# Performance work log

Measured on AMD Instinct MI355X. Metric: run time of the kernel, lower is better.

The kernel has to match this reference:

```python
import jax, jax.numpy as jnp
import numpy as np

ALPHA = 32.0 ** 2
EPS = 1e-5
SCALE = 64 ** (-0.5)  # dim_head ** -0.5
HEADS = 8


def stable_softmax(t, alpha=ALPHA):
    t = t / alpha
    t = t - jax.lax.stop_gradient(jnp.max(t, axis=-1, keepdims=True))
    return jax.nn.softmax(t * alpha, axis=-1)


def setup_inputs() -> dict:
    key = jax.random.key(0)
    k1, k2, k3 = jax.random.split(key, 3)
    dim, inner = 512, 8 * 64
    x = jax.random.normal(k1, (8, dim, 32, 32), dtype=jnp.float32)
    gamma = jnp.ones((1, dim, 1, 1), dtype=jnp.float32)
    # conv2d 1x1 weights, stored as [out_ch, in_ch]
    w_qkv = jax.random.normal(k2, (inner * 3, dim), dtype=jnp.float32) * (dim ** -0.5)
    w_out = jax.random.normal(k3, (dim, inner), dtype=jnp.float32) * (inner ** -0.5)
    return {"x": x, "gamma": gamma, "w_qkv": w_qkv, "w_out": w_out}


def reference(x, gamma, w_qkv, w_out):
    b, c, H, W = x.shape
    residual = x
    # LayerNormChan: normalize over channel dim (biased variance), scale by gamma
    mean = jnp.mean(x, axis=1, keepdims=True)
    var = jnp.var(x, axis=1, keepdims=True)
    xn = (x - mean) / jnp.sqrt(var + EPS) * gamma
    # 1x1 conv QKV projection
    qkv = jnp.einsum('oc,bchw->bohw', w_qkv, xn)
    q, k, v = jnp.split(qkv, 3, axis=1)
    n = H * W
    def to_heads(t):
        return t.reshape(b, HEADS, -1, n)  # b h c (x y)
    q, k, v = map(to_heads, (q, k, v))
    sim = jnp.einsum('bhci,bhcj->bhij', q, k) * SCALE
    attn = stable_softmax(sim)
    out = jnp.einsum('bhij,bhcj->bhci', attn, v)
    out = out.reshape(b, -1, H, W)  # b (h c) x y
    out = jnp.einsum('oc,bchw->bohw', w_out, out)
    return out + residual
```

## Files before the change

kernel.cpp:

```cpp
#include <hip/hip_runtime.h>
#include <hip/hip_bf16.h>

#define NDIM   512
#define NPOS   1024
#define NB     8
#define INNER  1536
#define DHEAD  64

typedef __attribute__((ext_vector_type(8))) short bf8v;
typedef __attribute__((ext_vector_type(4))) float f4v;

__device__ __forceinline__ f4v mfma16(bf8v a, bf8v b, f4v c) {
    return __builtin_amdgcn_mfma_f32_16x16x32_bf16(a, b, c, 0, 0, 0);
}

__device__ __forceinline__ unsigned short f2bs(float v) {
    __hip_bfloat16 h = __float2bfloat16(v);
    return *reinterpret_cast<unsigned short*>(&h);
}

__global__ __launch_bounds__(256) void ln_xnorm_kernel(
    const float* __restrict__ x, const float* __restrict__ gamma,
    unsigned short* __restrict__ xnT)
{
    __shared__ float ssum[4][64];
    __shared__ float ssq[4][64];
    __shared__ float mean_s[64];
    __shared__ float rstd_s[64];
    __shared__ unsigned short tile[64][72];

    const int b = blockIdx.y;
    const int n0 = blockIdx.x * 64;
    const int t = threadIdx.x;

    {
        const int ln = t & 63, cg = t >> 6;
        const float* xp = x + (size_t)b * NDIM * NPOS + n0 + ln;
        float s = 0.f, ss = 0.f;
        for (int c = cg * 128; c < cg * 128 + 128; ++c) {
            float v = xp[(size_t)c * NPOS];
            s += v; ss += v * v;
        }
        ssum[cg][ln] = s; ssq[cg][ln] = ss;
    }
    __syncthreads();
    if (t < 64) {
        float st = ssum[0][t] + ssum[1][t] + ssum[2][t] + ssum[3][t];
        float sq = ssq[0][t] + ssq[1][t] + ssq[2][t] + ssq[3][t];
        float m = st * (1.0f / NDIM);
        float var = sq * (1.0f / NDIM) - m * m;
        mean_s[t] = m;
        rstd_s[t] = rsqrtf(var + 1e-5f);
    }
    __syncthreads();

    const int cl = t >> 2, nq = (t & 3) * 16;
    const int n = t >> 2, cq = (t & 3) * 16;
    for (int c0 = 0; c0 < NDIM; c0 += 64) {
        const float g = gamma[c0 + cl];
        const float* xp = x + ((size_t)b * NDIM + c0 + cl) * NPOS + n0 + nq;
#pragma unroll
        for (int q = 0; q < 4; ++q) {
            float4 v = *(const float4*)(xp + q * 4);
            float4 m = *(const float4*)&mean_s[nq + q * 4];
            float4 r = *(const float4*)&rstd_s[nq + q * 4];
            tile[nq + q * 4 + 0][cl] = f2bs((v.x - m.x) * r.x * g);
            tile[nq + q * 4 + 1][cl] = f2bs((v.y - m.y) * r.y * g);
            tile[nq + q * 4 + 2][cl] = f2bs((v.z - m.z) * r.z * g);
            tile[nq + q * 4 + 3][cl] = f2bs((v.w - m.w) * r.w * g);
        }
        __syncthreads();
        unsigned short* dst = xnT + ((size_t)b * NPOS + n0 + n) * NDIM + c0 + cq;
        *(uint4*)dst       = *(const uint4*)&tile[n][cq];
        *(uint4*)(dst + 8) = *(const uint4*)&tile[n][cq + 8];
        __syncthreads();
    }
}

__global__ __launch_bounds__(256) void castw2_kernel(
    const float* __restrict__ wq, unsigned short* __restrict__ wqb,
    const float* __restrict__ wo, unsigned short* __restrict__ wob)
{
    const int n1 = INNER * NDIM / 4;
    int i = blockIdx.x * 256 + threadIdx.x;
    const float* src; unsigned short* dst; int j;
    if (i < n1) { src = wq; dst = wqb; j = i; }
    else        { src = wo; dst = wob; j = i - n1; }
    float4 v = ((const float4*)src)[j];
    ushort4 u;
    u.x = f2bs(v.x); u.y = f2bs(v.y); u.z = f2bs(v.z); u.w = f2bs(v.w);
    ((ushort4*)dst)[j] = u;
}

__global__ __launch_bounds__(256) void qkv_mfma_kernel(
    const unsigned short* __restrict__ wq, const unsigned short* __restrict__ xnT,
    unsigned short* __restrict__ qT, unsigned short* __restrict__ kT,
    unsigned short* __restrict__ vv)
{
    __shared__ unsigned short smem[4 * 64 * 72];
    unsigned short (*Al)[40] = (unsigned short(*)[40])smem;
    unsigned short (*Bl)[40] = (unsigned short(*)[40])(smem + 5120);

    const int b = blockIdx.z;
    const int m0 = blockIdx.y * 128, n0 = blockIdx.x * 128;
    const int t = threadIdx.x, w = t >> 6, lane = t & 63;
    const int l15 = lane & 15, quad = lane >> 4;
    const int wm = (w >> 1) * 64, wn = (w & 1) * 64;
    const unsigned short* Abase = wq + (size_t)m0 * NDIM;
    const unsigned short* Bbase = xnT + ((size_t)b * NPOS + n0) * NDIM;
    const int sr = t >> 1, sh = (t & 1) * 16;

    f4v acc[4][4];
#pragma unroll
    for (int i = 0; i < 4; ++i)
#pragma unroll
        for (int j = 0; j < 4; ++j) { acc[i][j][0]=0.f; acc[i][j][1]=0.f; acc[i][j][2]=0.f; acc[i][j][3]=0.f; }

    for (int k0 = 0; k0 < NDIM; k0 += 32) {
        uint4 a0 = *(const uint4*)(Abase + (size_t)sr * NDIM + k0 + sh);
        uint4 a1 = *(const uint4*)(Abase + (size_t)sr * NDIM + k0 + sh + 8);
        uint4 b0 = *(const uint4*)(Bbase + (size_t)sr * NDIM + k0 + sh);
        uint4 b1 = *(const uint4*)(Bbase + (size_t)sr * NDIM + k0 + sh + 8);
        __syncthreads();
        *(uint4*)&Al[sr][sh] = a0;  *(uint4*)&Al[sr][sh + 8] = a1;
        *(uint4*)&Bl[sr][sh] = b0;  *(uint4*)&Bl[sr][sh + 8] = b1;
        __syncthreads();
        bf8v af[4], bfr[4];
#pragma unroll
        for (int ms = 0; ms < 4; ++ms) af[ms]  = *(const bf8v*)&Al[wm + ms * 16 + l15][quad * 8];
#pragma unroll
        for (int ns = 0; ns < 4; ++ns) bfr[ns] = *(const bf8v*)&Bl[wn + ns * 16 + l15][quad * 8];
#pragma unroll
        for (int ms = 0; ms < 4; ++ms)
#pragma unroll
            for (int ns = 0; ns < 4; ++ns)
                acc[ms][ns] = mfma16(af[ms], bfr[ns], acc[ms][ns]);
    }
    __syncthreads();

    const int sec = m0 >> 9;
    const int om  = m0 & 511;
    if (sec == 2) {
        unsigned short* vbase = vv + ((size_t)b * NDIM + om) * NPOS + n0;
#pragma unroll
        for (int ms = 0; ms < 4; ++ms)
#pragma unroll
            for (int r = 0; r < 4; ++r) {
                int m = wm + ms * 16 + quad * 4 + r;
#pragma unroll
                for (int ns = 0; ns < 4; ++ns)
                    vbase[(size_t)m * NPOS + wn + ns * 16 + l15] = f2bs(acc[ms][ns][r]);
            }
    } else {
        const float qsc = (sec == 0) ? 0.125f : 1.0f;
        unsigned short* gT = (sec == 0 ? qT : kT) + ((size_t)b * NPOS + n0) * NDIM + om;
        unsigned short (*bw)[72] = (unsigned short(*)[72])(smem + w * 64 * 72);
#pragma unroll
        for (int ms = 0; ms < 4; ++ms)
#pragma unroll
            for (int ns = 0; ns < 4; ++ns)
#pragma unroll
                for (int r = 0; r < 4; ++r)
                    bw[ns * 16 + l15][ms * 16 + quad * 4 + r] = f2bs(acc[ms][ns][r] * qsc);
        unsigned short* dst = gT + (size_t)(wn + lane) * NDIM + wm;
#pragma unroll
        for (int q2 = 0; q2 < 8; ++q2)
            *(uint4*)(dst + q2 * 8) = *(const uint4*)&bw[lane][q2 * 8];
    }
}

__global__ __launch_bounds__(256) void attn_mfma3_kernel(
    const unsigned short* __restrict__ qT, const unsigned short* __restrict__ kT,
    const unsigned short* __restrict__ vv, unsigned short* __restrict__ attnT)
{
    __shared__ unsigned short Ks[64][72];
    __shared__ unsigned short Vs[80][72];
    __shared__ unsigned short Ps[4][32][72];

    const int blk = blockIdx.x;
    const int xg = blk & 7, rr = blk >> 3;
    const int i0 = (rr & 7) * 128;
    const int bh = ((rr >> 3) << 3) | xg;
    const int b = bh >> 3, h = bh & 7;

    const int t = threadIdx.x, w = t >> 6, lane = t & 63;
    const int l15 = lane & 15, quad = lane >> 4;

    const unsigned short* kbase = kT + (size_t)b * NPOS * NDIM + h * DHEAD;
    const unsigned short* vbase = vv + ((size_t)b * NDIM + h * DHEAD) * NPOS;

    bf8v bq[2][2];
#pragma unroll
    for (int g = 0; g < 2; ++g) {
        const unsigned short* qrow =
            qT + ((size_t)b * NPOS + i0 + w * 32 + g * 16 + l15) * NDIM + h * DHEAD;
        bq[g][0] = *(const bf8v*)(qrow + quad * 8);
        bq[g][1] = *(const bf8v*)(qrow + 32 + quad * 8);
    }

    {
        const int orow = 64 + (t >> 4), ocol = (t & 15) * 4;
        ushort4 one; one.x = one.y = one.z = one.w = 0x3F80;
        *(ushort4*)&Vs[orow][ocol] = one;
    }

    const int jr = t >> 2, cq = (t & 3) * 16;

    uint4 ka, kb2, va, vb2;
    {
        const unsigned short* kp = kbase + (size_t)jr * NDIM + cq;
        const unsigned short* vp = vbase + (size_t)jr * NPOS + cq;
        ka  = *(const uint4*)kp;  kb2 = *(const uint4*)(kp + 8);
        va  = *(const uint4*)vp;  vb2 = *(const uint4*)(vp + 8);
    }

    f4v oc[2][5];
#pragma unroll
    for (int mg = 0; mg < 2; ++mg)
#pragma unroll
        for (int cs = 0; cs < 5; ++cs) { oc[mg][cs][0]=0.f; oc[mg][cs][1]=0.f; oc[mg][cs][2]=0.f; oc[mg][cs][3]=0.f; }

    for (int j0 = 0; j0 < NPOS; j0 += 64) {
        __syncthreads();
        *(uint4*)&Ks[jr][cq] = ka;  *(uint4*)&Ks[jr][cq + 8] = kb2;
        *(uint4*)&Vs[jr][cq] = va;  *(uint4*)&Vs[jr][cq + 8] = vb2;
        __syncthreads();
        if (j0 + 64 < NPOS) {
            const unsigned short* kp = kbase + (size_t)(j0 + 64 + jr) * NDIM + cq;
            const unsigned short* vp = vbase + (size_t)jr * NPOS + j0 + 64 + cq;
            ka  = *(const uint4*)kp;  kb2 = *(const uint4*)(kp + 8);
            va  = *(const uint4*)vp;  vb2 = *(const uint4*)(vp + 8);
        }

#pragma unroll
        for (int jt = 0; jt < 4; ++jt) {
            bf8v ak0 = *(const bf8v*)&Ks[jt * 16 + l15][quad * 8];
            bf8v ak1 = *(const bf8v*)&Ks[jt * 16 + l15][32 + quad * 8];
#pragma unroll
            for (int g = 0; g < 2; ++g) {
                f4v s; s[0]=0.f; s[1]=0.f; s[2]=0.f; s[3]=0.f;
                s = mfma16(ak0, bq[g][0], s);
                s = mfma16(ak1, bq[g][1], s);
                ushort4 pu;
                pu.x = f2bs(__expf(fminf(s[0], 60.f)));
                pu.y = f2bs(__expf(fminf(s[1], 60.f)));
                pu.z = f2bs(__expf(fminf(s[2], 60.f)));
                pu.w = f2bs(__expf(fminf(s[3], 60.f)));
                *(ushort4*)&Ps[w][g * 16 + l15][jt * 16 + quad * 4] = pu;
            }
        }

        bf8v ap[2][2];
#pragma unroll
        for (int mg = 0; mg < 2; ++mg) {
            ap[mg][0] = *(const bf8v*)&Ps[w][mg * 16 + l15][quad * 8];
            ap[mg][1] = *(const bf8v*)&Ps[w][mg * 16 + l15][32 + quad * 8];
        }
#pragma unroll
        for (int cs = 0; cs < 5; ++cs) {
            bf8v bv0 = *(const bf8v*)&Vs[cs * 16 + l15][quad * 8];
            bf8v bv1 = *(const bf8v*)&Vs[cs * 16 + l15][32 + quad * 8];
#pragma unroll
            for (int mg = 0; mg < 2; ++mg) {
                oc[mg][cs] = mfma16(ap[mg][0], bv0, oc[mg][cs]);
                oc[mg][cs] = mfma16(ap[mg][1], bv1, oc[mg][cs]);
            }
        }
    }

#pragma unroll
    for (int mg = 0; mg < 2; ++mg) {
        float inv[4];
#pragma unroll
        for (int r = 0; r < 4; ++r) inv[r] = 1.0f / oc[mg][4][r];
        unsigned short* dst =
            attnT + ((size_t)b * NPOS + i0 + w * 32 + mg * 16) * NDIM + h * DHEAD;
#pragma unroll
        for (int cs = 0; cs < 4; ++cs)
#pragma unroll
            for (int r = 0; r < 4; ++r)
                dst[(size_t)(quad * 4 + r) * NDIM + cs * 16 + l15] = f2bs(oc[mg][cs][r] * inv[r]);
    }
}

__global__ __launch_bounds__(256) void out_mfma_kernel(
    const unsigned short* __restrict__ wo, const unsigned short* __restrict__ attnT,
    const float* __restrict__ x, float* __restrict__ outp)
{
    __shared__ unsigned short Al[128][40];
    __shared__ unsigned short Bl[128][40];
    const int b = blockIdx.z;
    const int m0 = blockIdx.y * 128, n0 = blockIdx.x * 128;
    const int t = threadIdx.x, w = t >> 6, lane = t & 63;
    const int l15 = lane & 15, quad = lane >> 4;
    const int wm = (w >> 1) * 64, wn = (w & 1) * 64;
    const unsigned short* Abase = wo + (size_t)m0 * NDIM;
    const unsigned short* Bbase = attnT + ((size_t)b * NPOS + n0) * NDIM;
    const int sr = t >> 1, sh = (t & 1) * 16;

    f4v acc[4][4];
#pragma unroll
    for (int i = 0; i < 4; ++i)
#pragma unroll
        for (int j = 0; j < 4; ++j) { acc[i][j][0]=0.f; acc[i][j][1]=0.f; acc[i][j][2]=0.f; acc[i][j][3]=0.f; }

    for (int k0 = 0; k0 < NDIM; k0 += 32) {
        uint4 a0 = *(const uint4*)(Abase + (size_t)sr * NDIM + k0 + sh);
        uint4 a1 = *(const uint4*)(Abase + (size_t)sr * NDIM + k0 + sh + 8);
        uint4 b0 = *(const uint4*)(Bbase + (size_t)sr * NDIM + k0 + sh);
        uint4 b1 = *(const uint4*)(Bbase + (size_t)sr * NDIM + k0 + sh + 8);
        __syncthreads();
        *(uint4*)&Al[sr][sh] = a0;  *(uint4*)&Al[sr][sh + 8] = a1;
        *(uint4*)&Bl[sr][sh] = b0;  *(uint4*)&Bl[sr][sh + 8] = b1;
        __syncthreads();
        bf8v af[4], bfr[4];
#pragma unroll
        for (int ms = 0; ms < 4; ++ms) af[ms]  = *(const bf8v*)&Al[wm + ms * 16 + l15][quad * 8];
#pragma unroll
        for (int ns = 0; ns < 4; ++ns) bfr[ns] = *(const bf8v*)&Bl[wn + ns * 16 + l15][quad * 8];
#pragma unroll
        for (int ms = 0; ms < 4; ++ms)
#pragma unroll
            for (int ns = 0; ns < 4; ++ns)
                acc[ms][ns] = mfma16(af[ms], bfr[ns], acc[ms][ns]);
    }
    const float* xb = x + ((size_t)b * NDIM + m0) * NPOS + n0;
    float* ob = outp + ((size_t)b * NDIM + m0) * NPOS + n0;
#pragma unroll
    for (int ms = 0; ms < 4; ++ms)
#pragma unroll
        for (int r = 0; r < 4; ++r) {
            int m = wm + ms * 16 + quad * 4 + r;
#pragma unroll
            for (int ns = 0; ns < 4; ++ns) {
                int n = wn + ns * 16 + l15;
                ob[(size_t)m * NPOS + n] = acc[ms][ns][r] + xb[(size_t)m * NPOS + n];
            }
        }
}

extern "C" void kernel_launch(void* const* d_in, const int* in_sizes, int n_in,
                              void* d_out, int out_size, void* d_ws, size_t ws_size,
                              hipStream_t stream) {
    const float* x     = (const float*)d_in[0];
    const float* gamma = (const float*)d_in[1];
    const float* w_qkv = (const float*)d_in[2];
    const float* w_out = (const float*)d_in[3];
    float* out = (float*)d_out;

    unsigned short* xnT = (unsigned short*)d_ws;
    unsigned short* wqb = xnT + (size_t)NB * NPOS * NDIM;
    unsigned short* wob = wqb + (size_t)INNER * NDIM;
    unsigned short* qTw = wob + (size_t)NDIM * NDIM;
    unsigned short* kTw = qTw + (size_t)NB * NPOS * NDIM;
    unsigned short* vvw = kTw + (size_t)NB * NPOS * NDIM;
    unsigned short* aTw = vvw + (size_t)NB * NPOS * NDIM;

    ln_xnorm_kernel<<<dim3(NPOS / 64, NB), 256, 0, stream>>>(x, gamma, xnT);
    castw2_kernel<<<(INNER * NDIM + NDIM * NDIM) / 4 / 256, 256, 0, stream>>>(
        w_qkv, wqb, w_out, wob);
    qkv_mfma_kernel<<<dim3(NPOS / 128, INNER / 128, NB), 256, 0, stream>>>(
        wqb, xnT, qTw, kTw, vvw);
    attn_mfma3_kernel<<<512, 256, 0, stream>>>(qTw, kTw, vvw, aTw);
    out_mfma_kernel<<<dim3(NPOS / 128, NDIM / 128, NB), 256, 0, stream>>>(wob, aTw, x, out);
}
```

Baseline: 164.4 us.

## Use direct global-to-LDS loads with XOR swizzle in GEMMs; drop LDS staging in attention

The QKV and output GEMMs now stage A/B tiles with global_load_lds (direct global-to-LDS DMA) into an unpadded layout with an XOR swizzle, so register staging and bank conflicts go away. The attention kernel no longer stages K and V through shared memory. Each wave reads K/V fragments straight from global memory (relying on L1/L2 reuse), and the ones-row used for the softmax denominator becomes a register constant. This removes two barriers per iteration in attention, at the cost of redundant global traffic across waves and lost prefetch overlap. The GEMMs also lose their register-level prefetch, since loads are now issued between the barriers.

```diff
diff --git a/kernel.cpp b/kernel.cpp
--- a/kernel.cpp
+++ b/kernel.cpp
@@ -17,6 +17,13 @@
 __device__ __forceinline__ unsigned short f2bs(float v) {
     __hip_bfloat16 h = __float2bfloat16(v);
     return *reinterpret_cast<unsigned short*>(&h);
+}
+
+__device__ __forceinline__ void gl_lds16(const unsigned short* g, unsigned short* l) {
+    __builtin_amdgcn_global_load_lds(
+        (const __attribute__((address_space(1))) void*)g,
+        (__attribute__((address_space(3))) void*)l,
+        16, 0, 0);
 }
 
 __global__ __launch_bounds__(256) void ln_xnorm_kernel(
@@ -97,9 +104,9 @@
     unsigned short* __restrict__ qT, unsigned short* __restrict__ kT,
     unsigned short* __restrict__ vv)
 {
-    __shared__ unsigned short smem[4 * 64 * 72];
-    unsigned short (*Al)[40] = (unsigned short(*)[40])smem;
-    unsigned short (*Bl)[40] = (unsigned short(*)[40])(smem + 5120);
+    __shared__ __align__(16) unsigned short smem[4 * 64 * 72];
+    unsigned short* At = smem;
+    unsigned short* Bt = smem + 4096;
 
     const int b = blockIdx.z;
     const int m0 = blockIdx.y * 128, n0 = blockIdx.x * 128;
@@ -108,7 +115,10 @@
     const int wm = (w >> 1) * 64, wn = (w & 1) * 64;
     const unsigned short* Abase = wq + (size_t)m0 * NDIM;
     const unsigned short* Bbase = xnT + ((size_t)b * NPOS + n0) * NDIM;
-    const int sr = t >> 1, sh = (t & 1) * 16;
+
+    const int rl = lane >> 2, sl = lane & 3;
+    const int cw = (sl ^ ((rl >> 1) & 3)) * 8;
+    const int sA = (quad ^ ((l15 >> 1) & 3)) * 8;
 
     f4v acc[4][4];
 #pragma unroll
@@ -117,19 +127,20 @@
         for (int j = 0; j < 4; ++j) { acc[i][j][0]=0.f; acc[i][j][1]=0.f; acc[i][j][2]=0.f; acc[i][j][3]=0.f; }
 
     for (int k0 = 0; k0 < NDIM; k0 += 32) {
-        uint4 a0 = *(const uint4*)(Abase + (size_t)sr * NDIM + k0 + sh);
-        uint4 a1 = *(const uint4*)(Abase + (size_t)sr * NDIM + k0 + sh + 8);
-        uint4 b0 = *(const uint4*)(Bbase + (size_t)sr * NDIM + k0 + sh);
-        uint4 b1 = *(const uint4*)(Bbase + (size_t)sr * NDIM + k0 + sh + 8);
-        __syncthreads();
-        *(uint4*)&Al[sr][sh] = a0;  *(uint4*)&Al[sr][sh + 8] = a1;
-        *(uint4*)&Bl[sr][sh] = b0;  *(uint4*)&Bl[sr][sh + 8] = b1;
+        __syncthreads();
+#pragma unroll
+        for (int e = 0; e < 2; ++e) {
+            const int seg = w * 2 + e;
+            const int r = seg * 16 + rl;
+            gl_lds16(Abase + (size_t)r * NDIM + k0 + cw, At + seg * 512);
+            gl_lds16(Bbase + (size_t)r * NDIM + k0 + cw, Bt + seg * 512);
+        }
         __syncthreads();
         bf8v af[4], bfr[4];
 #pragma unroll
-        for (int ms = 0; ms < 4; ++ms) af[ms]  = *(const bf8v*)&Al[wm + ms * 16 + l15][quad * 8];
-#pragma unroll
-        for (int ns = 0; ns < 4; ++ns) bfr[ns] = *(const bf8v*)&Bl[wn + ns * 16 + l15][quad * 8];
+        for (int ms = 0; ms < 4; ++ms) af[ms]  = *(const bf8v*)&At[(wm + ms * 16 + l15) * 32 + sA];
+#pragma unroll
+        for (int ns = 0; ns < 4; ++ns) bfr[ns] = *(const bf8v*)&Bt[(wn + ns * 16 + l15) * 32 + sA];
 #pragma unroll
         for (int ms = 0; ms < 4; ++ms)
 #pragma unroll
@@ -169,13 +180,11 @@
     }
 }
 
-__global__ __launch_bounds__(256) void attn_mfma3_kernel(
+__global__ __launch_bounds__(256) void attn_mfma4_kernel(
     const unsigned short* __restrict__ qT, const unsigned short* __restrict__ kT,
     const unsigned short* __restrict__ vv, unsigned short* __restrict__ attnT)
 {
-    __shared__ unsigned short Ks[64][72];
-    __shared__ unsigned short Vs[80][72];
-    __shared__ unsigned short Ps[4][32][72];
+    __shared__ __align__(16) unsigned short Ps[4][32][72];
 
     const int blk = blockIdx.x;
     const int xg = blk & 7, rr = blk >> 3;
@@ -198,21 +207,9 @@
         bq[g][1] = *(const bf8v*)(qrow + 32 + quad * 8);
     }
 
-    {
-        const int orow = 64 + (t >> 4), ocol = (t & 15) * 4;
-        ushort4 one; one.x = one.y = one.z = one.w = 0x3F80;
-        *(ushort4*)&Vs[orow][ocol] = one;
-    }
-
-    const int jr = t >> 2, cq = (t & 3) * 16;
-
-    uint4 ka, kb2, va, vb2;
-    {
-        const unsigned short* kp = kbase + (size_t)jr * NDIM + cq;
-        const unsigned short* vp = vbase + (size_t)jr * NPOS + cq;
-        ka  = *(const uint4*)kp;  kb2 = *(const uint4*)(kp + 8);
-        va  = *(const uint4*)vp;  vb2 = *(const uint4*)(vp + 8);
-    }
+    bf8v bones;
+#pragma unroll
+    for (int e = 0; e < 8; ++e) bones[e] = (short)0x3F80;
 
     f4v oc[2][5];
 #pragma unroll
@@ -221,21 +218,11 @@
         for (int cs = 0; cs < 5; ++cs) { oc[mg][cs][0]=0.f; oc[mg][cs][1]=0.f; oc[mg][cs][2]=0.f; oc[mg][cs][3]=0.f; }
 
     for (int j0 = 0; j0 < NPOS; j0 += 64) {
-        __syncthreads();
-        *(uint4*)&Ks[jr][cq] = ka;  *(uint4*)&Ks[jr][cq + 8] = kb2;
-        *(uint4*)&Vs[jr][cq] = va;  *(uint4*)&Vs[jr][cq + 8] = vb2;
-        __syncthreads();
-        if (j0 + 64 < NPOS) {
-            const unsigned short* kp = kbase + (size_t)(j0 + 64 + jr) * NDIM + cq;
-            const unsigned short* vp = vbase + (size_t)jr * NPOS + j0 + 64 + cq;
-            ka  = *(const uint4*)kp;  kb2 = *(const uint4*)(kp + 8);
-            va  = *(const uint4*)vp;  vb2 = *(const uint4*)(vp + 8);
-        }
-
 #pragma unroll
         for (int jt = 0; jt < 4; ++jt) {
-            bf8v ak0 = *(const bf8v*)&Ks[jt * 16 + l15][quad * 8];
-            bf8v ak1 = *(const bf8v*)&Ks[jt * 16 + l15][32 + quad * 8];
+            const unsigned short* krow = kbase + (size_t)(j0 + jt * 16 + l15) * NDIM;
+            bf8v ak0 = *(const bf8v*)(krow + quad * 8);
+            bf8v ak1 = *(const bf8v*)(krow + 32 + quad * 8);
 #pragma unroll
             for (int g = 0; g < 2; ++g) {
                 f4v s; s[0]=0.f; s[1]=0.f; s[2]=0.f; s[3]=0.f;
@@ -249,7 +236,6 @@
                 *(ushort4*)&Ps[w][g * 16 + l15][jt * 16 + quad * 4] = pu;
             }
         }
-
         bf8v ap[2][2];
 #pragma unroll
         for (int mg = 0; mg < 2; ++mg) {
@@ -257,15 +243,21 @@
             ap[mg][1] = *(const bf8v*)&Ps[w][mg * 16 + l15][32 + quad * 8];
         }
 #pragma unroll
-        for (int cs = 0; cs < 5; ++cs) {
-            bf8v bv0 = *(const bf8v*)&Vs[cs * 16 + l15][quad * 8];
-            bf8v bv1 = *(const bf8v*)&Vs[cs * 16 + l15][32 + quad * 8];
+        for (int cs = 0; cs < 4; ++cs) {
+            const unsigned short* vrow = vbase + (size_t)(cs * 16 + l15) * NPOS + j0;
+            bf8v bv0 = *(const bf8v*)(vrow + quad * 8);
+            bf8v bv1 = *(const bf8v*)(vrow + 32 + quad * 8);
 #pragma unroll
             for (int mg = 0; mg < 2; ++mg) {
                 oc[mg][cs] = mfma16(ap[mg][0], bv0, oc[mg][cs]);
                 oc[mg][cs] = mfma16(ap[mg][1], bv1, oc[mg][cs]);
             }
         }
+#pragma unroll
+        for (int mg = 0; mg < 2; ++mg) {
+            oc[mg][4] = mfma16(ap[mg][0], bones, oc[mg][4]);
+            oc[mg][4] = mfma16(ap[mg][1], bones, oc[mg][4]);
+        }
     }
 
 #pragma unroll
@@ -287,8 +279,10 @@
     const unsigned short* __restrict__ wo, const unsigned short* __restrict__ attnT,
     const float* __restrict__ x, float* __restrict__ outp)
 {
-    __shared__ unsigned short Al[128][40];
-    __shared__ unsigned short Bl[128][40];
+    __shared__ __align__(16) unsigned short smem[8192];
+    unsigned short* At = smem;
+    unsigned short* Bt = smem + 4096;
+
     const int b = blockIdx.z;
     const int m0 = blockIdx.y * 128, n0 = blockIdx.x * 128;
     const int t = threadIdx.x, w = t >> 6, lane = t & 63;
@@ -296,7 +290,10 @@
     const int wm = (w >> 1) * 64, wn = (w & 1) * 64;
     const unsigned short* Abase = wo + (size_t)m0 * NDIM;
     const unsigned short* Bbase = attnT + ((size_t)b * NPOS + n0) * NDIM;
-    const int sr = t >> 1, sh = (t & 1) * 16;
+
+    const int rl = lane >> 2, sl = lane & 3;
+    const int cw = (sl ^ ((rl >> 1) & 3)) * 8;
+    const int sA = (quad ^ ((l15 >> 1) & 3)) * 8;
 
     f4v acc[4][4];
 #pragma unroll
@@ -305,19 +302,20 @@
         for (int j = 0; j < 4; ++j) { acc[i][j][0]=0.f; acc[i][j][1]=0.f; acc[i][j][2]=0.f; acc[i][j][3]=0.f; }
 
     for (int k0 = 0; k0 < NDIM; k0 += 32) {
-        uint4 a0 = *(const uint4*)(Abase + (size_t)sr * NDIM + k0 + sh);
-        uint4 a1 = *(const uint4*)(Abase + (size_t)sr * NDIM + k0 + sh + 8);
-        uint4 b0 = *(const uint4*)(Bbase + (size_t)sr * NDIM + k0 + sh);
-        uint4 b1 = *(const uint4*)(Bbase + (size_t)sr * NDIM + k0 + sh + 8);
-        __syncthreads();
-        *(uint4*)&Al[sr][sh] = a0;  *(uint4*)&Al[sr][sh + 8] = a1;
-        *(uint4*)&Bl[sr][sh] = b0;  *(uint4*)&Bl[sr][sh + 8] = b1;
+        __syncthreads();
+#pragma unroll
+        for (int e = 0; e < 2; ++e) {
+            const int seg = w * 2 + e;
+            const int r = seg * 16 + rl;
+            gl_lds16(Abase + (size_t)r * NDIM + k0 + cw, At + seg * 512);
+            gl_lds16(Bbase + (size_t)r * NDIM + k0 + cw, Bt + seg * 512);
+        }
         __syncthreads();
         bf8v af[4], bfr[4];
 #pragma unroll
-        for (int ms = 0; ms < 4; ++ms) af[ms]  = *(const bf8v*)&Al[wm + ms * 16 + l15][quad * 8];
-#pragma unroll
-        for (int ns = 0; ns < 4; ++ns) bfr[ns] = *(const bf8v*)&Bl[wn + ns * 16 + l15][quad * 8];
+        for (int ms = 0; ms < 4; ++ms) af[ms]  = *(const bf8v*)&At[(wm + ms * 16 + l15) * 32 + sA];
+#pragma unroll
+        for (int ns = 0; ns < 4; ++ns) bfr[ns] = *(const bf8v*)&Bt[(wn + ns * 16 + l15) * 32 + sA];
 #pragma unroll
         for (int ms = 0; ms < 4; ++ms)
 #pragma unroll
@@ -361,6 +359,6 @@
         w_qkv, wqb, w_out, wob);
     qkv_mfma_kernel<<<dim3(NPOS / 128, INNER / 128, NB), 256, 0, stream>>>(
         wqb, xnT, qTw, kTw, vvw);
-    attn_mfma3_kernel<<<512, 256, 0, stream>>>(qTw, kTw, vvw, aTw);
+    attn_mfma4_kernel<<<512, 256, 0, stream>>>(qTw, kTw, vvw, aTw);
     out_mfma_kernel<<<dim3(NPOS / 128, NDIM / 128, NB), 256, 0, stream>>>(wob, aTw, x, out);
 }
```

After: 185.1 us. +12.6%, slower.
